# Performance work log

Hardware: AMD Instinct MI355X
Metric: run time of the kernel (lower is better)

## Reference

```python
import jax, jax.numpy as jnp
import numpy as np

NEG_SLOPE = 0.2


def gat_layer(x, W, a_src, a_dst, b, src, dst, num_nodes, heads, out_c, concat):
    # Linear transform per head: [N, heads, out_c]
    h = (x @ W).reshape(num_nodes, heads, out_c)
    # Per-node attention logits for source/dest roles: [N, heads]
    e_src = jnp.einsum('nhc,hc->nh', h, a_src)
    e_dst = jnp.einsum('nhc,hc->nh', h, a_dst)
    # Edge-wise scores (gather), LeakyReLU: [E, heads]
    e = jax.nn.leaky_relu(e_src[src] + e_dst[dst], negative_slope=NEG_SLOPE)
    # Segment softmax over incoming edges of each destination node
    m = jax.ops.segment_max(e, dst, num_segments=num_nodes)
    ex = jnp.exp(e - m[dst])
    denom = jax.ops.segment_sum(ex, dst, num_segments=num_nodes)
    alpha = ex / denom[dst]                       # [E, heads]
    # Weighted scatter-aggregate of source messages: [N, heads, out_c]
    out = jax.ops.segment_sum(h[src] * alpha[:, :, None], dst, num_segments=num_nodes)
    if concat:
        out = out.reshape(num_nodes, heads * out_c)
    else:
        out = out.mean(axis=1)
    return out + b


def setup_inputs() -> dict:
    key = jax.random.key(0)
    ks = jax.random.split(key, 12)
    N, E = 50000, 800000
    in_c, out_c, heads = 128, 32, 4
    x = jax.random.normal(ks[0], (N, in_c), dtype=jnp.float32)
    edge_index = jax.random.randint(ks[1], (2, E), 0, N, dtype=jnp.int64)
    s1 = 1.0 / np.sqrt(in_c)
    W1 = jax.random.normal(ks[2], (in_c, heads * out_c), dtype=jnp.float32) * s1
    a_src1 = jax.random.normal(ks[3], (heads, out_c), dtype=jnp.float32) * 0.1
    a_dst1 = jax.random.normal(ks[4], (heads, out_c), dtype=jnp.float32) * 0.1
    b1 = jnp.zeros((heads * out_c,), dtype=jnp.float32)
    s2 = 1.0 / np.sqrt(heads * out_c)
    W2 = jax.random.normal(ks[5], (heads * out_c, out_c), dtype=jnp.float32) * s2
    a_src2 = jax.random.normal(ks[6], (1, out_c), dtype=jnp.float32) * 0.1
    a_dst2 = jax.random.normal(ks[7], (1, out_c), dtype=jnp.float32) * 0.1
    b2 = jnp.zeros((out_c,), dtype=jnp.float32)
    return {"x": x, "edge_index": edge_index, "W1": W1, "a_src1": a_src1,
            "a_dst1": a_dst1, "b1": b1, "W2": W2, "a_src2": a_src2,
            "a_dst2": a_dst2, "b2": b2}


def reference(x, edge_index, W1, a_src1, a_dst1, b1, W2, a_src2, a_dst2, b2):
    N = x.shape[0]
    heads, out_c = a_src1.shape
    # add_self_loops=True (PyG default)
    loops = jnp.arange(N, dtype=edge_index.dtype)
    src = jnp.concatenate([edge_index[0], loops])
    dst = jnp.concatenate([edge_index[1], loops])
    h1 = gat_layer(x, W1, a_src1, a_dst1, b1, src, dst, N, heads, out_c, concat=True)
    h1 = jax.nn.elu(h1)
    out = gat_layer(h1, W2, a_src2, a_dst2, b2, src, dst, N, 1, out_c, concat=False)
    return out
```

## Files before the change

kernel.cpp:

```cpp
#include <hip/hip_runtime.h>
#include <hip/hip_bf16.h>

#define LRELU_SLOPE 0.2f
#define NB_SHIFT 7

typedef __attribute__((ext_vector_type(8))) short short8;
typedef __attribute__((ext_vector_type(4))) float float4v;

__device__ inline float b2f(unsigned short u) {
    union { unsigned int i; float f; } v; v.i = ((unsigned int)u) << 16; return v.f;
}
__device__ inline unsigned short f2b(float f) {
    union { float f; unsigned int i; } v; v.f = f;
    unsigned int x = v.i;
    unsigned int r = x + 0x7fffu + ((x >> 16) & 1u);
    return (unsigned short)(r >> 16);
}
__device__ inline float lrelu(float x) { return x > 0.f ? x : LRELU_SLOPE * x; }

__global__ __launch_bounds__(256) void hist_kernel(const int* __restrict__ dst,
                                                   int E, int Etot, int nb, int nblk,
                                                   int chunk, int* __restrict__ cnt) {
    __shared__ int hist[512];
    int blk = blockIdx.x;
    for (int i = threadIdx.x; i < nb; i += 256) hist[i] = 0;
    __syncthreads();
    int lo = blk * chunk;
    int hi = lo + chunk; if (hi > Etot) hi = Etot;
    for (int i = lo + threadIdx.x; i < hi; i += 256) {
        int d = (i < E) ? dst[i] : (i - E);
        atomicAdd(&hist[d >> NB_SHIFT], 1);
    }
    __syncthreads();
    for (int b = threadIdx.x; b < nb; b += 256)
        cnt[b * nblk + blk] = hist[b];
}

__global__ __launch_bounds__(1024) void scanA_kernel(int* cnt, int* bsum, int M) {
    __shared__ int tile[1024];
    int i = blockIdx.x * 1024 + threadIdx.x;
    int v = (i < M) ? cnt[i] : 0;
    tile[threadIdx.x] = v;
    __syncthreads();
    for (int off = 1; off < 1024; off <<= 1) {
        int t = (threadIdx.x >= (unsigned)off) ? tile[threadIdx.x - off] : 0;
        __syncthreads();
        tile[threadIdx.x] += t;
        __syncthreads();
    }
    int incl = tile[threadIdx.x];
    if (i < M) cnt[i] = incl - v;
    if (threadIdx.x == 1023) bsum[blockIdx.x] = incl;
}

__global__ __launch_bounds__(256) void scanB_kernel(int* __restrict__ bsum, int nb) {
    __shared__ int tile[256];
    int v = (threadIdx.x < (unsigned)nb) ? bsum[threadIdx.x] : 0;
    tile[threadIdx.x] = v;
    __syncthreads();
    for (int off = 1; off < 256; off <<= 1) {
        int t = (threadIdx.x >= (unsigned)off) ? tile[threadIdx.x - off] : 0;
        __syncthreads();
        tile[threadIdx.x] += t;
        __syncthreads();
    }
    if (threadIdx.x < (unsigned)nb) bsum[threadIdx.x] = tile[threadIdx.x] - v;
}

__global__ __launch_bounds__(256) void partition_kernel(
        const int* __restrict__ src, const int* __restrict__ dst,
        int E, int Etot, int nb, int nblk, int chunk,
        const int* __restrict__ cnt, const int* __restrict__ boff,
        int2* __restrict__ bkt) {
    __shared__ int cur[512];
    int blk = blockIdx.x;
    for (int b = threadIdx.x; b < nb; b += 256) {
        int idx = b * nblk + blk;
        cur[b] = cnt[idx] + boff[idx >> 10];
    }
    __syncthreads();
    int lo = blk * chunk;
    int hi = lo + chunk; if (hi > Etot) hi = Etot;
    for (int i = lo + threadIdx.x; i < hi; i += 256) {
        int s, d;
        if (i < E) { s = src[i]; d = dst[i]; }
        else       { s = d = i - E; }
        int pos = atomicAdd(&cur[d >> NB_SHIFT], 1);
        bkt[pos] = make_int2(s, d);
    }
}

__global__ __launch_bounds__(256) void finalize_kernel(
        const int2* __restrict__ bkt, const int* __restrict__ cnt,
        const int* __restrict__ boff, int nb, int nblk,
        const float* __restrict__ es, const float* __restrict__ ed,
        int* __restrict__ ptr, int* __restrict__ csr_src, float* __restrict__ w1,
        int N, int Etot) {
    __shared__ int deg[128];
    __shared__ int scn[128];
    __shared__ int cur[128];
    int b = blockIdx.x;
    int idx0 = b * nblk;
    int base = cnt[idx0] + boff[idx0 >> 10];
    int nextbase;
    if (b + 1 < nb) {
        int idx1 = (b + 1) * nblk;
        nextbase = cnt[idx1] + boff[idx1 >> 10];
    } else nextbase = Etot;
    int count = nextbase - base;
    int node0 = b << NB_SHIFT;
    int nodes = N - node0; if (nodes > 128) nodes = 128;

    if (threadIdx.x < 128) deg[threadIdx.x] = 0;
    __syncthreads();
    for (int i = threadIdx.x; i < count; i += 256)
        atomicAdd(&deg[bkt[base + i].y - node0], 1);
    __syncthreads();
    int v = (threadIdx.x < 128) ? deg[threadIdx.x] : 0;
    if (threadIdx.x < 128) scn[threadIdx.x] = v;
    __syncthreads();
    for (int off = 1; off < 128; off <<= 1) {
        int t = (threadIdx.x < 128 && threadIdx.x >= (unsigned)off) ? scn[threadIdx.x - off] : 0;
        __syncthreads();
        if (threadIdx.x < 128) scn[threadIdx.x] += t;
        __syncthreads();
    }
    if (threadIdx.x < 128) {
        int excl = scn[threadIdx.x] - v;
        cur[threadIdx.x] = excl;
        if (threadIdx.x < nodes) ptr[node0 + threadIdx.x] = base + excl;
    }
    if (b == nb - 1 && threadIdx.x == 0) ptr[N] = Etot;
    __syncthreads();
    for (int i = threadIdx.x; i < count; i += 256) {
        int2 sd = bkt[base + i];
        int pos = base + atomicAdd(&cur[sd.y - node0], 1);
        csr_src[pos] = sd.x;
        float4 a = *(const float4*)&es[sd.x * 4];
        float4 bb = *(const float4*)&ed[sd.y * 4];
        float4 ww;
        ww.x = __expf(lrelu(a.x + bb.x));
        ww.y = __expf(lrelu(a.y + bb.y));
        ww.z = __expf(lrelu(a.z + bb.z));
        ww.w = __expf(lrelu(a.w + bb.w));
        *(float4*)&w1[(size_t)pos * 4] = ww;
    }
}

__global__ __launch_bounds__(256) void gemm1_mfma_kernel(
        const float* __restrict__ x, const float* __restrict__ W1,
        const float* __restrict__ a_src, const float* __restrict__ a_dst,
        unsigned short* __restrict__ h1b, float* __restrict__ es,
        float* __restrict__ ed, int N) {
    __shared__ unsigned short xs[64][136];
    __shared__ unsigned short wt[128][136];
    int tid = threadIdx.x;
    int n0 = blockIdx.x * 64;

    for (int i = tid; i < 128 * 128; i += 256) {
        int k = i >> 7, n = i & 127;
        wt[n][k] = f2b(W1[i]);
    }
    for (int i = tid; i < 64 * 128; i += 256) {
        int r = i >> 7, k = i & 127;
        int row = n0 + r; if (row >= N) row = N - 1;
        xs[r][k] = f2b(x[(size_t)row * 128 + k]);
    }
    __syncthreads();

    int wave = tid >> 6;
    int lane = tid & 63;
    int lrow = lane & 15;
    int quad = lane >> 4;

    short8 afr[4];
#pragma unroll
    for (int kc = 0; kc < 4; kc++)
        afr[kc] = *(const short8*)&xs[wave * 16 + lrow][kc * 32 + quad * 8];
    __syncthreads();

#pragma unroll
    for (int ct = 0; ct < 8; ct++) {
        float4v acc = {0.f, 0.f, 0.f, 0.f};
#pragma unroll
        for (int kc = 0; kc < 4; kc++) {
            short8 bfr = *(const short8*)&wt[ct * 16 + lrow][kc * 32 + quad * 8];
            acc = __builtin_amdgcn_mfma_f32_16x16x32_bf16(afr[kc], bfr, acc, 0, 0, 0);
        }
#pragma unroll
        for (int r = 0; r < 4; r++) {
            int lr = wave * 16 + quad * 4 + r;
            int grow = n0 + lr;
            unsigned short hb = f2b(acc[r]);
            xs[lr][ct * 16 + lrow] = hb;
            if (grow < N)
                h1b[grow * 128 + ct * 16 + lrow] = hb;
        }
    }
    __syncthreads();

    int row = tid >> 2, h = tid & 3;
    int rg = n0 + row;
    if (rg < N) {
        const float* ap = a_src + h * 32;
        const float* bp = a_dst + h * 32;
        float s = 0.f, d = 0.f;
#pragma unroll
        for (int c2 = 0; c2 < 16; c2++) {
            unsigned int u = *(const unsigned int*)&xs[row][h * 32 + 2 * c2];
            float v0 = b2f((unsigned short)(u & 0xffffu));
            float v1 = b2f((unsigned short)(u >> 16));
            float2 a = *(const float2*)&ap[2 * c2];
            float2 b = *(const float2*)&bp[2 * c2];
            s += v0 * a.x + v1 * a.y;
            d += v0 * b.x + v1 * b.y;
        }
        es[rg * 4 + h] = s;
        ed[rg * 4 + h] = d;
    }
}

__global__ __launch_bounds__(256) void gemm2_mfma_kernel(
        const unsigned short* __restrict__ h1e, const float* __restrict__ W2,
        const float* __restrict__ a_src, const float* __restrict__ a_dst,
        unsigned short* __restrict__ h2b, float* __restrict__ es,
        float* __restrict__ ed, int N) {
    __shared__ unsigned short xs[64][136];
    __shared__ unsigned short wt[32][136];
    int tid = threadIdx.x;
    int n0 = blockIdx.x * 64;

    for (int i = tid; i < 128 * 32; i += 256) {
        int k = i >> 5, n = i & 31;
        wt[n][k] = f2b(W2[i]);
    }
    {
        const unsigned int* srcp = (const unsigned int*)(h1e + (size_t)n0 * 128);
        int rows = (N - n0) < 64 ? (N - n0) : 64;
        int maxu = rows * 64;
        for (int i = tid; i < 4096; i += 256) {
            unsigned int v = (i < maxu) ? srcp[i] : 0u;
            int r = i >> 6, cp = (i & 63) << 1;
            *(unsigned int*)&xs[r][cp] = v;
        }
    }
    __syncthreads();

    int wave = tid >> 6;
    int lane = tid & 63;
    int lrow = lane & 15;
    int quad = lane >> 4;

    short8 afr[4];
#pragma unroll
    for (int kc = 0; kc < 4; kc++)
        afr[kc] = *(const short8*)&xs[wave * 16 + lrow][kc * 32 + quad * 8];
    __syncthreads();

#pragma unroll
    for (int ct = 0; ct < 2; ct++) {
        float4v acc = {0.f, 0.f, 0.f, 0.f};
#pragma unroll
        for (int kc = 0; kc < 4; kc++) {
            short8 bfr = *(const short8*)&wt[ct * 16 + lrow][kc * 32 + quad * 8];
            acc = __builtin_amdgcn_mfma_f32_16x16x32_bf16(afr[kc], bfr, acc, 0, 0, 0);
        }
#pragma unroll
        for (int r = 0; r < 4; r++) {
            int lr = wave * 16 + quad * 4 + r;
            int grow = n0 + lr;
            unsigned short hb = f2b(acc[r]);
            xs[lr][ct * 16 + lrow] = hb;
            if (grow < N)
                h2b[(size_t)grow * 32 + ct * 16 + lrow] = hb;
        }
    }
    __syncthreads();

    if (tid < 64) {
        int rg = n0 + tid;
        if (rg < N) {
            float s = 0.f, d = 0.f;
#pragma unroll
            for (int c2 = 0; c2 < 16; c2++) {
                unsigned int u = *(const unsigned int*)&xs[tid][2 * c2];
                float v0 = b2f((unsigned short)(u & 0xffffu));
                float v1 = b2f((unsigned short)(u >> 16));
                float2 a = *(const float2*)&a_src[2 * c2];
                float2 b = *(const float2*)&a_dst[2 * c2];
                s += v0 * a.x + v1 * a.y;
                d += v0 * b.x + v1 * b.y;
            }
            es[rg] = s;
            ed[rg] = d;
        }
    }
}

__global__ __launch_bounds__(256) void agg1_kernel(
        const unsigned int* __restrict__ h1u, const float* __restrict__ w1,
        const int* __restrict__ csr, const int* __restrict__ ptr,
        const float* __restrict__ b1, unsigned int* __restrict__ h1e_u, int N) {
    int wave = threadIdx.x >> 6;
    int lane = threadIdx.x & 63;
    int n = blockIdx.x * 4 + wave;
    if (n >= N) return;
    int h = lane >> 4;
    int start = ptr[n], end = ptr[n + 1];
    float acc0 = 0.f, acc1 = 0.f, wsum = 0.f;
    int i = start;
    for (; i + 8 <= end; i += 8) {
        int s[8]; float v[8]; unsigned int g[8];
#pragma unroll
        for (int k = 0; k < 8; k++) s[k] = csr[i + k];
#pragma unroll
        for (int k = 0; k < 8; k++) v[k] = w1[(size_t)(i + k) * 4 + h];
#pragma unroll
        for (int k = 0; k < 8; k++) g[k] = h1u[(s[k] << 6) + lane];
#pragma unroll
        for (int k = 0; k < 8; k++) {
            acc0 += v[k] * b2f((unsigned short)(g[k] & 0xffffu));
            acc1 += v[k] * b2f((unsigned short)(g[k] >> 16));
            wsum += v[k];
        }
    }
    for (; i + 4 <= end; i += 4) {
        int s[4]; float v[4]; unsigned int g[4];
#pragma unroll
        for (int k = 0; k < 4; k++) s[k] = csr[i + k];
#pragma unroll
        for (int k = 0; k < 4; k++) v[k] = w1[(size_t)(i + k) * 4 + h];
#pragma unroll
        for (int k = 0; k < 4; k++) g[k] = h1u[(s[k] << 6) + lane];
#pragma unroll
        for (int k = 0; k < 4; k++) {
            acc0 += v[k] * b2f((unsigned short)(g[k] & 0xffffu));
            acc1 += v[k] * b2f((unsigned short)(g[k] >> 16));
            wsum += v[k];
        }
    }
    for (; i < end; i++) {
        int s = csr[i];
        float v = w1[(size_t)i * 4 + h];
        unsigned int g = h1u[(s << 6) + lane];
        acc0 += v * b2f((unsigned short)(g & 0xffffu));
        acc1 += v * b2f((unsigned short)(g >> 16));
        wsum += v;
    }
    float r = 1.f / wsum;
    float2 bb = ((const float2*)b1)[lane];
    float o0 = acc0 * r + bb.x;
    float o1 = acc1 * r + bb.y;
    o0 = o0 > 0.f ? o0 : __expf(o0) - 1.f;
    o1 = o1 > 0.f ? o1 : __expf(o1) - 1.f;
    h1e_u[(n << 6) + lane] = (unsigned int)f2b(o0) | ((unsigned int)f2b(o1) << 16);
}

__global__ __launch_bounds__(256) void agg2_kernel(
        const unsigned int* __restrict__ h2u, const float* __restrict__ es,
        const float* __restrict__ ed, const int* __restrict__ csr,
        const int* __restrict__ ptr, const float* __restrict__ b2,
        float* __restrict__ out, int N) {
    int lane = threadIdx.x & 63;
    int n = blockIdx.x * 16 + (threadIdx.x >> 6) * 4 + (lane >> 4);
    if (n >= N) return;
    int cl = lane & 15;
    float edl = ed[n];
    int start = ptr[n], end = ptr[n + 1];
    float acc0 = 0.f, acc1 = 0.f, wsum = 0.f;
    int i = start;
    for (; i + 4 <= end; i += 4) {
        int s[4]; float e[4]; unsigned int g[4];
#pragma unroll
        for (int k = 0; k < 4; k++) s[k] = csr[i + k];
#pragma unroll
        for (int k = 0; k < 4; k++) e[k] = es[s[k]];
#pragma unroll
        for (int k = 0; k < 4; k++) g[k] = h2u[(s[k] << 4) + cl];
#pragma unroll
        for (int k = 0; k < 4; k++) {
            float v = __expf(lrelu(e[k] + edl));
            acc0 += v * b2f((unsigned short)(g[k] & 0xffffu));
            acc1 += v * b2f((unsigned short)(g[k] >> 16));
            wsum += v;
        }
    }
    for (; i < end; i++) {
        int s = csr[i];
        float v = __expf(lrelu(es[s] + edl));
        unsigned int g = h2u[(s << 4) + cl];
        acc0 += v * b2f((unsigned short)(g & 0xffffu));
        acc1 += v * b2f((unsigned short)(g >> 16));
        wsum += v;
    }
    float r = 1.f / wsum;
    float2 bb = ((const float2*)b2)[cl];
    float2 o;
    o.x = acc0 * r + bb.x;
    o.y = acc1 * r + bb.y;
    ((float2*)out)[(size_t)n * 16 + cl] = o;
}

extern "C" void kernel_launch(void* const* d_in, const int* in_sizes, int n_in,
                              void* d_out, int out_size, void* d_ws, size_t ws_size,
                              hipStream_t stream) {
    const float* x      = (const float*)d_in[0];
    const int*   ei     = (const int*)  d_in[1];
    const float* W1     = (const float*)d_in[2];
    const float* a_src1 = (const float*)d_in[3];
    const float* a_dst1 = (const float*)d_in[4];
    const float* b1     = (const float*)d_in[5];
    const float* W2     = (const float*)d_in[6];
    const float* a_src2 = (const float*)d_in[7];
    const float* a_dst2 = (const float*)d_in[8];
    const float* b2     = (const float*)d_in[9];
    float* outp = (float*)d_out;

    const int N = in_sizes[0] / 128;
    const int E = in_sizes[1] / 2;
    const int Etot = E + N;

    const int* src = ei;
    const int* dst = ei + E;

    const int nb   = (N + 127) >> 7;
    const int nblk = 128;
    const int chunk = (Etot + nblk - 1) / nblk;
    const int M = nb * nblk;
    const int nbA = (M + 1023) / 1024;

    char* w = (char*)d_ws;
    unsigned short* h1b = (unsigned short*)(w + 0);
    unsigned short* h1e = (unsigned short*)(w + 12800000);
    unsigned short* h2b = (unsigned short*)(w + 25600000);
    float* es1  = (float*)(w + 28800000);
    float* ed1  = (float*)(w + 29600000);
    float* es2  = (float*)(w + 30400000);
    float* ed2  = (float*)(w + 30600000);
    int*   ptr  = (int*)  (w + 30800000);
    int*   bsum = (int*)  (w + 31000064);
    int*   cnt  = (int*)  (w + 31001088);
    int*   csr_src = (int*)(w + 31201280);
    int2*  bkt  = (int2*) (w + 34601280);
    float* w1   = (float*)(w + 41401280);

    gemm1_mfma_kernel<<<(N + 63) / 64, 256, 0, stream>>>(x, W1, a_src1, a_dst1,
                                                         h1b, es1, ed1, N);

    hist_kernel<<<nblk, 256, 0, stream>>>(dst, E, Etot, nb, nblk, chunk, cnt);
    scanA_kernel<<<nbA, 1024, 0, stream>>>(cnt, bsum, M);
    scanB_kernel<<<1, 256, 0, stream>>>(bsum, nbA);
    partition_kernel<<<nblk, 256, 0, stream>>>(src, dst, E, Etot, nb, nblk, chunk,
                                               cnt, bsum, bkt);
    finalize_kernel<<<nb, 256, 0, stream>>>(bkt, cnt, bsum, nb, nblk, es1, ed1,
                                            ptr, csr_src, w1, N, Etot);

    agg1_kernel<<<(N + 3) / 4, 256, 0, stream>>>((const unsigned int*)h1b, w1,
                                                 csr_src, ptr, b1,
                                                 (unsigned int*)h1e, N);

    gemm2_mfma_kernel<<<(N + 63) / 64, 256, 0, stream>>>(h1e, W2, a_src2, a_dst2,
                                                         h2b, es2, ed2, N);
    agg2_kernel<<<(N + 15) / 16, 256, 0, stream>>>((const unsigned int*)h2b, es2, ed2,
                                                   csr_src, ptr, b2, outp, N);
}
```

Before: 217.3 us.

## Fuse histogram into GEMM1, widen partition grid, fp16 edge weights, half-wave agg1

Merges the edge-destination histogram into the first GEMM kernel, reusing the weight tile's shared memory, and runs it on 512 blocks instead of 128 to spread the counting and partition work. Edge attention weights are stored as fp16 instead of fp32 to halve that traffic. agg1 now handles each node with 32 lanes loading 8-byte vectors, eight nodes per block, and its 4-edge unrolled tail is removed. Costs are a larger count array to scan, lower precision in the edge weights, and fewer parallel edge gathers in flight per node.

```diff
diff --git a/kernel.cpp b/kernel.cpp
--- a/kernel.cpp
+++ b/kernel.cpp
@@ -3,6 +3,7 @@
 
 #define LRELU_SLOPE 0.2f
 #define NB_SHIFT 7
+#define NBLK 512
 
 typedef __attribute__((ext_vector_type(8))) short short8;
 typedef __attribute__((ext_vector_type(4))) float float4v;
@@ -18,22 +19,97 @@
 }
 __device__ inline float lrelu(float x) { return x > 0.f ? x : LRELU_SLOPE * x; }
 
-__global__ __launch_bounds__(256) void hist_kernel(const int* __restrict__ dst,
-                                                   int E, int Etot, int nb, int nblk,
-                                                   int chunk, int* __restrict__ cnt) {
-    __shared__ int hist[512];
+__global__ __launch_bounds__(256) void gemm1_mfma_kernel(
+        const float* __restrict__ x, const float* __restrict__ W1,
+        const float* __restrict__ a_src, const float* __restrict__ a_dst,
+        unsigned short* __restrict__ h1b, float* __restrict__ es,
+        float* __restrict__ ed, int N,
+        const int* __restrict__ dst, int E, int Etot, int nb, int chunk,
+        int* __restrict__ cnt) {
+    __shared__ unsigned short xs[64][136];
+    __shared__ unsigned short wt[128][136];
+    int tid = threadIdx.x;
+    int n0 = blockIdx.x * 64;
+
+    for (int i = tid; i < 128 * 128; i += 256) {
+        int k = i >> 7, n = i & 127;
+        wt[n][k] = f2b(W1[i]);
+    }
+    for (int i = tid; i < 64 * 128; i += 256) {
+        int r = i >> 7, k = i & 127;
+        int row = n0 + r; if (row >= N) row = N - 1;
+        xs[r][k] = f2b(x[(size_t)row * 128 + k]);
+    }
+    __syncthreads();
+
+    int wave = tid >> 6;
+    int lane = tid & 63;
+    int lrow = lane & 15;
+    int quad = lane >> 4;
+
+    short8 afr[4];
+#pragma unroll
+    for (int kc = 0; kc < 4; kc++)
+        afr[kc] = *(const short8*)&xs[wave * 16 + lrow][kc * 32 + quad * 8];
+    __syncthreads();
+
+#pragma unroll
+    for (int ct = 0; ct < 8; ct++) {
+        float4v acc = {0.f, 0.f, 0.f, 0.f};
+#pragma unroll
+        for (int kc = 0; kc < 4; kc++) {
+            short8 bfr = *(const short8*)&wt[ct * 16 + lrow][kc * 32 + quad * 8];
+            acc = __builtin_amdgcn_mfma_f32_16x16x32_bf16(afr[kc], bfr, acc, 0, 0, 0);
+        }
+#pragma unroll
+        for (int r = 0; r < 4; r++) {
+            int lr = wave * 16 + quad * 4 + r;
+            int grow = n0 + lr;
+            unsigned short hb = f2b(acc[r]);
+            xs[lr][ct * 16 + lrow] = hb;
+            if (grow < N)
+                h1b[grow * 128 + ct * 16 + lrow] = hb;
+        }
+    }
+    __syncthreads();
+
+    int row = tid >> 2, h = tid & 3;
+    int rg = n0 + row;
+    if (rg < N) {
+        const float* ap = a_src + h * 32;
+        const float* bp = a_dst + h * 32;
+        float s = 0.f, d = 0.f;
+#pragma unroll
+        for (int c2 = 0; c2 < 16; c2++) {
+            unsigned int u = *(const unsigned int*)&xs[row][h * 32 + 2 * c2];
+            float v0 = b2f((unsigned short)(u & 0xffffu));
+            float v1 = b2f((unsigned short)(u >> 16));
+            float2 a = *(const float2*)&ap[2 * c2];
+            float2 b = *(const float2*)&bp[2 * c2];
+            s += v0 * a.x + v1 * a.y;
+            d += v0 * b.x + v1 * b.y;
+        }
+        es[rg * 4 + h] = s;
+        ed[rg * 4 + h] = d;
+    }
+
+    int* histm = (int*)&wt[0][0];
     int blk = blockIdx.x;
-    for (int i = threadIdx.x; i < nb; i += 256) hist[i] = 0;
-    __syncthreads();
-    int lo = blk * chunk;
-    int hi = lo + chunk; if (hi > Etot) hi = Etot;
-    for (int i = lo + threadIdx.x; i < hi; i += 256) {
-        int d = (i < E) ? dst[i] : (i - E);
-        atomicAdd(&hist[d >> NB_SHIFT], 1);
-    }
-    __syncthreads();
-    for (int b = threadIdx.x; b < nb; b += 256)
-        cnt[b * nblk + blk] = hist[b];
+    if (blk < NBLK)
+        for (int i = tid; i < nb; i += 256) histm[i] = 0;
+    __syncthreads();
+    if (blk < NBLK) {
+        int lo = blk * chunk;
+        int hi = lo + chunk; if (hi > Etot) hi = Etot;
+        for (int i = lo + tid; i < hi; i += 256) {
+            int d = (i < E) ? dst[i] : (i - E);
+            atomicAdd(&histm[d >> NB_SHIFT], 1);
+        }
+    }
+    __syncthreads();
+    if (blk < NBLK)
+        for (int b = tid; b < nb; b += 256)
+            cnt[b * NBLK + blk] = histm[b];
 }
 
 __global__ __launch_bounds__(1024) void scanA_kernel(int* cnt, int* bsum, int M) {
@@ -69,13 +145,13 @@
 
 __global__ __launch_bounds__(256) void partition_kernel(
         const int* __restrict__ src, const int* __restrict__ dst,
-        int E, int Etot, int nb, int nblk, int chunk,
+        int E, int Etot, int nb, int chunk,
         const int* __restrict__ cnt, const int* __restrict__ boff,
         int2* __restrict__ bkt) {
     __shared__ int cur[512];
     int blk = blockIdx.x;
     for (int b = threadIdx.x; b < nb; b += 256) {
-        int idx = b * nblk + blk;
+        int idx = b * NBLK + blk;
         cur[b] = cnt[idx] + boff[idx >> 10];
     }
     __syncthreads();
@@ -92,19 +168,19 @@
 
 __global__ __launch_bounds__(256) void finalize_kernel(
         const int2* __restrict__ bkt, const int* __restrict__ cnt,
-        const int* __restrict__ boff, int nb, int nblk,
+        const int* __restrict__ boff, int nb,
         const float* __restrict__ es, const float* __restrict__ ed,
-        int* __restrict__ ptr, int* __restrict__ csr_src, float* __restrict__ w1,
-        int N, int Etot) {
+        int* __restrict__ ptr, int* __restrict__ csr_src,
+        _Float16* __restrict__ w1h, int N, int Etot) {
     __shared__ int deg[128];
     __shared__ int scn[128];
     __shared__ int cur[128];
     int b = blockIdx.x;
-    int idx0 = b * nblk;
+    int idx0 = b * NBLK;
     int base = cnt[idx0] + boff[idx0 >> 10];
     int nextbase;
     if (b + 1 < nb) {
-        int idx1 = (b + 1) * nblk;
+        int idx1 = (b + 1) * NBLK;
         nextbase = cnt[idx1] + boff[idx1 >> 10];
     } else nextbase = Etot;
     int count = nextbase - base;
@@ -138,85 +214,12 @@
         csr_src[pos] = sd.x;
         float4 a = *(const float4*)&es[sd.x * 4];
         float4 bb = *(const float4*)&ed[sd.y * 4];
-        float4 ww;
-        ww.x = __expf(lrelu(a.x + bb.x));
-        ww.y = __expf(lrelu(a.y + bb.y));
-        ww.z = __expf(lrelu(a.z + bb.z));
-        ww.w = __expf(lrelu(a.w + bb.w));
-        *(float4*)&w1[(size_t)pos * 4] = ww;
-    }
-}
-
-__global__ __launch_bounds__(256) void gemm1_mfma_kernel(
-        const float* __restrict__ x, const float* __restrict__ W1,
-        const float* __restrict__ a_src, const float* __restrict__ a_dst,
-        unsigned short* __restrict__ h1b, float* __restrict__ es,
-        float* __restrict__ ed, int N) {
-    __shared__ unsigned short xs[64][136];
-    __shared__ unsigned short wt[128][136];
-    int tid = threadIdx.x;
-    int n0 = blockIdx.x * 64;
-
-    for (int i = tid; i < 128 * 128; i += 256) {
-        int k = i >> 7, n = i & 127;
-        wt[n][k] = f2b(W1[i]);
-    }
-    for (int i = tid; i < 64 * 128; i += 256) {
-        int r = i >> 7, k = i & 127;
-        int row = n0 + r; if (row >= N) row = N - 1;
-        xs[r][k] = f2b(x[(size_t)row * 128 + k]);
-    }
-    __syncthreads();
-
-    int wave = tid >> 6;
-    int lane = tid & 63;
-    int lrow = lane & 15;
-    int quad = lane >> 4;
-
-    short8 afr[4];
-#pragma unroll
-    for (int kc = 0; kc < 4; kc++)
-        afr[kc] = *(const short8*)&xs[wave * 16 + lrow][kc * 32 + quad * 8];
-    __syncthreads();
-
-#pragma unroll
-    for (int ct = 0; ct < 8; ct++) {
-        float4v acc = {0.f, 0.f, 0.f, 0.f};
-#pragma unroll
-        for (int kc = 0; kc < 4; kc++) {
-            short8 bfr = *(const short8*)&wt[ct * 16 + lrow][kc * 32 + quad * 8];
-            acc = __builtin_amdgcn_mfma_f32_16x16x32_bf16(afr[kc], bfr, acc, 0, 0, 0);
-        }
-#pragma unroll
-        for (int r = 0; r < 4; r++) {
-            int lr = wave * 16 + quad * 4 + r;
-            int grow = n0 + lr;
-            unsigned short hb = f2b(acc[r]);
-            xs[lr][ct * 16 + lrow] = hb;
-            if (grow < N)
-                h1b[grow * 128 + ct * 16 + lrow] = hb;
-        }
-    }
-    __syncthreads();
-
-    int row = tid >> 2, h = tid & 3;
-    int rg = n0 + row;
-    if (rg < N) {
-        const float* ap = a_src + h * 32;
-        const float* bp = a_dst + h * 32;
-        float s = 0.f, d = 0.f;
-#pragma unroll
-        for (int c2 = 0; c2 < 16; c2++) {
-            unsigned int u = *(const unsigned int*)&xs[row][h * 32 + 2 * c2];
-            float v0 = b2f((unsigned short)(u & 0xffffu));
-            float v1 = b2f((unsigned short)(u >> 16));
-            float2 a = *(const float2*)&ap[2 * c2];
-            float2 b = *(const float2*)&bp[2 * c2];
-            s += v0 * a.x + v1 * a.y;
-            d += v0 * b.x + v1 * b.y;
-        }
-        es[rg * 4 + h] = s;
-        ed[rg * 4 + h] = d;
+        union { _Float16 h[4]; uint2 u; } ww;
+        ww.h[0] = (_Float16)__expf(lrelu(a.x + bb.x));
+        ww.h[1] = (_Float16)__expf(lrelu(a.y + bb.y));
+        ww.h[2] = (_Float16)__expf(lrelu(a.z + bb.z));
+        ww.h[3] = (_Float16)__expf(lrelu(a.w + bb.w));
+        *(uint2*)&w1h[(size_t)pos * 4] = ww.u;
     }
 }
 
@@ -298,62 +301,58 @@
 }
 
 __global__ __launch_bounds__(256) void agg1_kernel(
-        const unsigned int* __restrict__ h1u, const float* __restrict__ w1,
+        const uint2* __restrict__ h1v, const _Float16* __restrict__ w1h,
         const int* __restrict__ csr, const int* __restrict__ ptr,
-        const float* __restrict__ b1, unsigned int* __restrict__ h1e_u, int N) {
-    int wave = threadIdx.x >> 6;
-    int lane = threadIdx.x & 63;
-    int n = blockIdx.x * 4 + wave;
+        const float* __restrict__ b1, uint2* __restrict__ h1e_v, int N) {
+    int tid = threadIdx.x;
+    int n = blockIdx.x * 8 + (tid >> 5);
     if (n >= N) return;
-    int h = lane >> 4;
+    int cl = tid & 31;
+    int h = cl >> 3;
     int start = ptr[n], end = ptr[n + 1];
-    float acc0 = 0.f, acc1 = 0.f, wsum = 0.f;
+    float a0 = 0.f, a1 = 0.f, a2 = 0.f, a3 = 0.f, ws = 0.f;
     int i = start;
     for (; i + 8 <= end; i += 8) {
-        int s[8]; float v[8]; unsigned int g[8];
+        int s[8]; float v[8]; uint2 g[8];
 #pragma unroll
         for (int k = 0; k < 8; k++) s[k] = csr[i + k];
 #pragma unroll
-        for (int k = 0; k < 8; k++) v[k] = w1[(size_t)(i + k) * 4 + h];
-#pragma unroll
-        for (int k = 0; k < 8; k++) g[k] = h1u[(s[k] << 6) + lane];
+        for (int k = 0; k < 8; k++) v[k] = (float)w1h[(size_t)(i + k) * 4 + h];
+#pragma unroll
+        for (int k = 0; k < 8; k++) g[k] = h1v[(s[k] << 5) + cl];
 #pragma unroll
         for (int k = 0; k < 8; k++) {
-            acc0 += v[k] * b2f((unsigned short)(g[k] & 0xffffu));
-            acc1 += v[k] * b2f((unsigned short)(g[k] >> 16));
-            wsum += v[k];
-        }
-    }
-    for (; i + 4 <= end; i += 4) {
-        int s[4]; float v[4]; unsigned int g[4];
-#pragma unroll
-        for (int k = 0; k < 4; k++) s[k] = csr[i + k];
-#pragma unroll
-        for (int k = 0; k < 4; k++) v[k] = w1[(size_t)(i + k) * 4 + h];
-#pragma unroll
-        for (int k = 0; k < 4; k++) g[k] = h1u[(s[k] << 6) + lane];
-#pragma unroll
-        for (int k = 0; k < 4; k++) {
-            acc0 += v[k] * b2f((unsigned short)(g[k] & 0xffffu));
-            acc1 += v[k] * b2f((unsigned short)(g[k] >> 16));
-            wsum += v[k];
+            a0 += v[k] * b2f((unsigned short)(g[k].x & 0xffffu));
+            a1 += v[k] * b2f((unsigned short)(g[k].x >> 16));
+            a2 += v[k] * b2f((unsigned short)(g[k].y & 0xffffu));
+            a3 += v[k] * b2f((unsigned short)(g[k].y >> 16));
+            ws += v[k];
         }
     }
     for (; i < end; i++) {
         int s = csr[i];
-        float v = w1[(size_t)i * 4 + h];
-        unsigned int g = h1u[(s << 6) + lane];
-        acc0 += v * b2f((unsigned short)(g & 0xffffu));
-        acc1 += v * b2f((unsigned short)(g >> 16));
-        wsum += v;
-    }
-    float r = 1.f / wsum;
-    float2 bb = ((const float2*)b1)[lane];
-    float o0 = acc0 * r + bb.x;
-    float o1 = acc1 * r + bb.y;
+        float v = (float)w1h[(size_t)i * 4 + h];
+        uint2 g = h1v[(s << 5) + cl];
+        a0 += v * b2f((unsigned short)(g.x & 0xffffu));
+        a1 += v * b2f((unsigned short)(g.x >> 16));
+        a2 += v * b2f((unsigned short)(g.y & 0xffffu));
+        a3 += v * b2f((unsigned short)(g.y >> 16));
+        ws += v;
+    }
+    float r = 1.f / ws;
+    float4 bb = ((const float4*)b1)[cl];
+    float o0 = a0 * r + bb.x;
+    float o1 = a1 * r + bb.y;
+    float o2 = a2 * r + bb.z;
+    float o3 = a3 * r + bb.w;
     o0 = o0 > 0.f ? o0 : __expf(o0) - 1.f;
     o1 = o1 > 0.f ? o1 : __expf(o1) - 1.f;
-    h1e_u[(n << 6) + lane] = (unsigned int)f2b(o0) | ((unsigned int)f2b(o1) << 16);
+    o2 = o2 > 0.f ? o2 : __expf(o2) - 1.f;
+    o3 = o3 > 0.f ? o3 : __expf(o3) - 1.f;
+    uint2 outv;
+    outv.x = (unsigned int)f2b(o0) | ((unsigned int)f2b(o1) << 16);
+    outv.y = (unsigned int)f2b(o2) | ((unsigned int)f2b(o3) << 16);
+    h1e_v[(n << 5) + cl] = outv;
 }
 
 __global__ __launch_bounds__(256) void agg2_kernel(
@@ -423,10 +422,9 @@
     const int* src = ei;
     const int* dst = ei + E;
 
-    const int nb   = (N + 127) >> 7;
-    const int nblk = 128;
-    const int chunk = (Etot + nblk - 1) / nblk;
-    const int M = nb * nblk;
+    const int nb    = (N + 127) >> 7;
+    const int chunk = (Etot + NBLK - 1) / NBLK;
+    const int M = nb * NBLK;
     const int nbA = (M + 1023) / 1024;
 
     char* w = (char*)d_ws;
@@ -440,24 +438,24 @@
     int*   ptr  = (int*)  (w + 30800000);
     int*   bsum = (int*)  (w + 31000064);
     int*   cnt  = (int*)  (w + 31001088);
-    int*   csr_src = (int*)(w + 31201280);
-    int2*  bkt  = (int2*) (w + 34601280);
-    float* w1   = (float*)(w + 41401280);
+    int*   csr_src = (int*)(w + 31801856);
+    int2*  bkt  = (int2*) (w + 35201856);
+    _Float16* w1h = (_Float16*)(w + 42001856);
 
     gemm1_mfma_kernel<<<(N + 63) / 64, 256, 0, stream>>>(x, W1, a_src1, a_dst1,
-                                                         h1b, es1, ed1, N);
-
-    hist_kernel<<<nblk, 256, 0, stream>>>(dst, E, Etot, nb, nblk, chunk, cnt);
+                                                         h1b, es1, ed1, N,
+                                                         dst, E, Etot, nb, chunk, cnt);
+
     scanA_kernel<<<nbA, 1024, 0, stream>>>(cnt, bsum, M);
     scanB_kernel<<<1, 256, 0, stream>>>(bsum, nbA);
-    partition_kernel<<<nblk, 256, 0, stream>>>(src, dst, E, Etot, nb, nblk, chunk,
+    partition_kernel<<<NBLK, 256, 0, stream>>>(src, dst, E, Etot, nb, chunk,
                                                cnt, bsum, bkt);
-    finalize_kernel<<<nb, 256, 0, stream>>>(bkt, cnt, bsum, nb, nblk, es1, ed1,
-                                            ptr, csr_src, w1, N, Etot);
-
-    agg1_kernel<<<(N + 3) / 4, 256, 0, stream>>>((const unsigned int*)h1b, w1,
+    finalize_kernel<<<nb, 256, 0, stream>>>(bkt, cnt, bsum, nb, es1, ed1,
+                                            ptr, csr_src, w1h, N, Etot);
+
+    agg1_kernel<<<(N + 7) / 8, 256, 0, stream>>>((const uint2*)h1b, w1h,
                                                  csr_src, ptr, b1,
-                                                 (unsigned int*)h1e, N);
+                                                 (uint2*)h1e, N);
 
     gemm2_mfma_kernel<<<(N + 63) / 64, 256, 0, stream>>>(h1e, W2, a_src2, a_dst2,
                                                          h2b, es2, ed2, N);
```

New measurement: 201.0 us. 7.5% less time.
